# Kernel tuning notes

Hardware: AMD Instinct MI355X
Metric: run time of the kernel (lower is better)

The kernel has to match this reference:

```python
import jax, jax.numpy as jnp
import numpy as np

EPS = 1e-5

def _gru(m, h, wih, whh, bih, bhh):
    gi = m @ wih.T + bih
    gh = h @ whh.T + bhh
    ir, iz, inn = jnp.split(gi, 3, axis=-1)
    hr, hz, hn = jnp.split(gh, 3, axis=-1)
    r = jax.nn.sigmoid(ir + hr)
    z = jax.nn.sigmoid(iz + hz)
    n = jnp.tanh(inn + r * hn)
    return (1.0 - z) * n + z * h

def _mggc(h, src, dst, etype, coeff, w, wih, whh, bih, bhh, num_nodes):
    # w: [L, T, C, C]; per-edge-type linear transform, scatter-add aggregation, GRU update
    for l in range(w.shape[0]):
        tr = jnp.einsum('nc,tcd->tnd', h, w[l])            # [T, N, C]
        msg = tr[etype, src] * coeff[src][:, None]          # [E, C] gather by (edge type, source)
        aggr = jax.ops.segment_sum(msg, dst, num_segments=num_nodes)
        h = _gru(aggr, h, wih, whh, bih, bhh)
    return h

def _bn(x, g, b):
    mu = x.mean(axis=0)
    var = x.var(axis=0)
    return (x - mu) * jax.lax.rsqrt(var + EPS) * g + b

def _lstm_cell(inp, h, c, wih, whh, b):
    gates = inp @ wih.T + h @ whh.T + b
    i, f, g, o = jnp.split(gates, 4, axis=-1)
    c = jax.nn.sigmoid(f) * c + jax.nn.sigmoid(i) * jnp.tanh(g)
    h = jax.nn.sigmoid(o) * jnp.tanh(c)
    return h, c

def _set2set(x, batch, num_graphs, wih0, whh0, b0, wih1, whh1, b1, steps=5):
    C = x.shape[1]
    B = num_graphs
    q_star = jnp.zeros((B, 2 * C), x.dtype)
    h0 = jnp.zeros((B, C), x.dtype); c0 = h0; h1 = h0; c1 = h0
    for _ in range(steps):
        h0, c0 = _lstm_cell(q_star, h0, c0, wih0, whh0, b0)
        h1, c1 = _lstm_cell(h0, h1, c1, wih1, whh1, b1)
        q = h1                                              # [B, C]
        e = jnp.sum(x * q[batch], axis=-1)                  # [N]
        emax = jax.ops.segment_max(e, batch, num_segments=B)
        ex = jnp.exp(e - emax[batch])
        denom = jax.ops.segment_sum(ex, batch, num_segments=B)
        a = ex / denom[batch]                               # scatter-softmax over graphs
        r = jax.ops.segment_sum(a[:, None] * x, batch, num_segments=B)
        q_star = jnp.concatenate([q, r], axis=1)
    return q_star                                           # [B, 2C]

def _forward(x, edge_attr, conv_w, conv_wih, conv_whh, conv_bih, conv_bhh, conv_nt,
             s2s1_wih0, s2s1_whh0, s2s1_b0, s2s1_wih1, s2s1_whh1, s2s1_b1,
             s2s2_wih0, s2s2_whh0, s2s2_b0, s2s2_wih1, s2s2_whh1, s2s2_b1,
             bn_g, bn_b, prebn_g, prebn_b,
             fc_w0, fc_b0, fc_w1, fc_b1, fc_w2, fc_b2,
             fcbn_g0, fcbn_b0, fcbn_g1, fcbn_b1,
             edge_index, node_type, batch, assign_src, assign_dst, edge_index_2, batch_2, num_graphs):
    N = x.shape[0]
    N2 = batch_2.shape[0]
    etype = jnp.argmax(edge_attr[:, :4], axis=1)           # edge type from one-hot part of edge_attr
    src, dst = edge_index[0], edge_index[1]
    h = x
    for i in range(3):
        coeff = conv_nt[i][node_type]                      # per-node-type coefficient
        h = _mggc(h, src, dst, etype, coeff, conv_w[i], conv_wih[i], conv_whh[i], conv_bih[i], conv_bhh[i], N)
        h = jax.nn.relu(_bn(h, bn_g[i], bn_b[i]))
    x1 = _set2set(h, batch, num_graphs, s2s1_wih0, s2s1_whh0, s2s1_b0, s2s1_wih1, s2s1_whh1, s2s1_b1)
    # avg_pool: mean of level-1 node features into level-2 clusters
    cnt = jax.ops.segment_sum(jnp.ones((assign_dst.shape[0],), x.dtype), assign_dst, num_segments=N2)
    h2 = jax.ops.segment_sum(h[assign_src], assign_dst, num_segments=N2) / jnp.maximum(cnt, 1.0)[:, None]
    src2, dst2 = edge_index_2[0], edge_index_2[1]
    etype2 = jnp.zeros((src2.shape[0],), jnp.int32)
    ones2 = jnp.ones((N2,), x.dtype)
    h2 = jax.nn.relu(_mggc(h2, src2, dst2, etype2, ones2, conv_w[3], conv_wih[3], conv_whh[3], conv_bih[3], conv_bhh[3], N2))
    h2 = jax.nn.relu(_mggc(h2, src2, dst2, etype2, ones2, conv_w[4], conv_wih[4], conv_whh[4], conv_bih[4], conv_bhh[4], N2))
    x2 = _set2set(h2, batch_2, num_graphs, s2s2_wih0, s2s2_whh0, s2s2_b0, s2s2_wih1, s2s2_whh1, s2s2_b1)
    z = jnp.concatenate([x1, x2], axis=1)                  # [B, 4C] = [B, 256]
    z = _bn(z, prebn_g, prebn_b)
    z = jax.nn.relu(_bn(z @ fc_w0.T + fc_b0, fcbn_g0, fcbn_b0))  # dropout: eval-mode identity
    z = jax.nn.relu(_bn(z @ fc_w1.T + fc_b1, fcbn_g1, fcbn_b1))
    return z @ fc_w2.T + fc_b2                             # [B, 1]

def setup_inputs() -> dict:
    C, L, T, NT = 64, 3, 4, 9
    N, E, N2, E2, A, B = 60000, 600000, 20000, 150000, 60000, 256
    key = jax.random.key(0)
    ks = iter(jax.random.split(key, 48))
    nrm = lambda shape, s: jax.random.normal(next(ks), shape, jnp.float32) * s
    inp = {}
    inp['x'] = nrm((N, C), 1.0)
    inp['edge_attr'] = jax.random.uniform(next(ks), (E, 10), jnp.float32)
    inp['conv_w'] = nrm((5, L, T, C, C), 0.125)
    inp['conv_wih'] = nrm((5, 3 * C, C), 0.125)
    inp['conv_whh'] = nrm((5, 3 * C, C), 0.125)
    inp['conv_bih'] = jnp.zeros((5, 3 * C), jnp.float32)
    inp['conv_bhh'] = jnp.zeros((5, 3 * C), jnp.float32)
    inp['conv_nt'] = 1.0 + nrm((5, NT), 0.1)
    for nm in ('s2s1', 's2s2'):
        inp[nm + '_wih0'] = nrm((4 * C, 2 * C), 0.09)
        inp[nm + '_whh0'] = nrm((4 * C, C), 0.125)
        inp[nm + '_b0'] = jnp.zeros((4 * C,), jnp.float32)
        inp[nm + '_wih1'] = nrm((4 * C, C), 0.125)
        inp[nm + '_whh1'] = nrm((4 * C, C), 0.125)
        inp[nm + '_b1'] = jnp.zeros((4 * C,), jnp.float32)
    inp['bn_g'] = jnp.ones((3, C), jnp.float32)
    inp['bn_b'] = jnp.zeros((3, C), jnp.float32)
    inp['prebn_g'] = jnp.ones((4 * C,), jnp.float32)
    inp['prebn_b'] = jnp.zeros((4 * C,), jnp.float32)
    inp['fc_w0'] = nrm((128, 256), 0.0625)
    inp['fc_b0'] = jnp.zeros((128,), jnp.float32)
    inp['fc_w1'] = nrm((64, 128), 0.09)
    inp['fc_b1'] = jnp.zeros((64,), jnp.float32)
    inp['fc_w2'] = nrm((1, 64), 0.125)
    inp['fc_b2'] = jnp.zeros((1,), jnp.float32)
    inp['fcbn_g0'] = jnp.ones((128,), jnp.float32)
    inp['fcbn_b0'] = jnp.zeros((128,), jnp.float32)
    inp['fcbn_g1'] = jnp.ones((64,), jnp.float32)
    inp['fcbn_b1'] = jnp.zeros((64,), jnp.float32)
    inp['edge_index'] = jax.random.randint(next(ks), (2, E), 0, N)
    inp['node_type'] = jax.random.randint(next(ks), (N,), 0, NT)
    inp['batch'] = jnp.sort(jax.random.randint(next(ks), (N,), 0, B))
    inp['assign_src'] = jax.random.randint(next(ks), (A,), 0, N)
    inp['assign_dst'] = jax.random.randint(next(ks), (A,), 0, N2)
    inp['edge_index_2'] = jax.random.randint(next(ks), (2, E2), 0, N2)
    inp['batch_2'] = jnp.sort(jax.random.randint(next(ks), (N2,), 0, B))
    inp['num_graphs'] = B
    return inp

def reference(x, edge_attr, conv_w, conv_wih, conv_whh, conv_bih, conv_bhh, conv_nt,
              s2s1_wih0, s2s1_whh0, s2s1_b0, s2s1_wih1, s2s1_whh1, s2s1_b1,
              s2s2_wih0, s2s2_whh0, s2s2_b0, s2s2_wih1, s2s2_whh1, s2s2_b1,
              bn_g, bn_b, prebn_g, prebn_b,
              fc_w0, fc_b0, fc_w1, fc_b1, fc_w2, fc_b2,
              fcbn_g0, fcbn_b0, fcbn_g1, fcbn_b1,
              edge_index, node_type, batch, assign_src, assign_dst, edge_index_2, batch_2, num_graphs):
    return _forward(x, edge_attr, conv_w, conv_wih, conv_whh, conv_bih, conv_bhh, conv_nt,
                    s2s1_wih0, s2s1_whh0, s2s1_b0, s2s1_wih1, s2s1_whh1, s2s1_b1,
                    s2s2_wih0, s2s2_whh0, s2s2_b0, s2s2_wih1, s2s2_whh1, s2s2_b1,
                    bn_g, bn_b, prebn_g, prebn_b,
                    fc_w0, fc_b0, fc_w1, fc_b1, fc_w2, fc_b2,
                    fcbn_g0, fcbn_b0, fcbn_g1, fcbn_b1,
                    edge_index, node_type, batch, assign_src, assign_dst, edge_index_2, batch_2, num_graphs)
```

## Files before the change

kernel.cpp:

```cpp
#include <hip/hip_runtime.h>

#define NN1 60000
#define EE1 600000
#define NN2 20000
#define EE2 150000
#define AA  60000

__device__ __forceinline__ float sigf(float x){ return 1.f/(1.f+expf(-x)); }
__device__ __forceinline__ float rlane(float v, int sl){
  return __int_as_float(__builtin_amdgcn_readlane(__float_as_int(v), sl));
}
#define RL4(SL) hx = rlane(ld.x, SL); hy = rlane(ld.y, SL); hz = rlane(ld.z, SL); hw = rlane(ld.w, SL);
#define FMA4(A, W) A = fmaf(hx, W.x, A); A = fmaf(hy, W.y, A); A = fmaf(hz, W.z, A); A = fmaf(hw, W.w, A);

__global__ void k_relu(float* a, int n){
  int i = blockIdx.x*blockDim.x + threadIdx.x;
  if (i < n) a[i] = fmaxf(a[i], 0.f);
}
__global__ void k_copy(const float* __restrict__ a, float* __restrict__ o, int n){
  int i = blockIdx.x*blockDim.x + threadIdx.x;
  if (i < n) o[i] = a[i];
}

__global__ void k_etype(const float* __restrict__ ea, int* __restrict__ etype, int E){
  int e = blockIdx.x*blockDim.x + threadIdx.x;
  if (e >= E) return;
  const float* p = ea + (size_t)e*10;
  float best = p[0]; int bi = 0;
  #pragma unroll
  for (int k = 1; k < 4; ++k){ float v = p[k]; if (v > best){ best = v; bi = k; } }
  etype[e] = bi;
}

__global__ void k_coeff(const float* __restrict__ nt, const int* __restrict__ node_type,
                        float* __restrict__ coeff, int N){
  int n = blockIdx.x*blockDim.x + threadIdx.x;
  if (n < N) coeff[n] = nt[node_type[n]];
}

__global__ void k_batchptr(const int* __restrict__ batch, int* __restrict__ rb, int N, int B){
  int n = blockIdx.x*blockDim.x + threadIdx.x;
  if (n >= N) return;
  int b = batch[n];
  if (n == 0){ for (int g = 0; g <= b; ++g) rb[g] = 0; }
  else {
    int pb = batch[n-1];
    for (int g = pb+1; g <= b; ++g) rb[g] = n;
  }
  if (n == N-1){ for (int g = b+1; g <= B; ++g) rb[g] = N; }
}

__global__ void k_prep_msgw(const float* __restrict__ w, float* __restrict__ w4){
  int idx = blockIdx.x*256 + threadIdx.x;
  if (idx >= 245760) return;
  int m = idx >> 12, r = idx & 4095;
  int c4 = r >> 8, d = (r >> 2) & 63, q = r & 3;
  w4[idx] = w[m*4096 + (4*c4+q)*64 + d];
}
__global__ void k_prep_gruw(const float* __restrict__ wih, const float* __restrict__ whh,
                            float* __restrict__ wihT, float* __restrict__ wihW,
                            float* __restrict__ whh4){
  int idx = blockIdx.x*256 + threadIdx.x;
  if (idx >= 61440) return;
  {
    int l = idx / 12288, r = idx % 12288;
    int t = r >> 12, rr = r & 4095;
    int c4 = rr >> 8, d = (rr >> 2) & 63, q = rr & 3;
    wihT[idx] = wih[l*12288 + (64*t + d)*64 + 4*c4 + q];
  }
  {
    int l = idx / 12288, rr = idx % 12288;
    int e = rr >> 2, q = rr & 3;
    int c4 = e / 192, j = e - c4*192;
    wihW[idx] = wih[l*12288 + j*64 + 4*c4 + q];
    whh4[idx] = whh[l*12288 + j*64 + 4*c4 + q];
  }
}

__global__ void k_s2strans(const float* __restrict__ wih0, const float* __restrict__ whh0,
                           const float* __restrict__ wih1, const float* __restrict__ whh1,
                           float* __restrict__ T){
  int idx = blockIdx.x*256 + threadIdx.x;
  if (idx < 32768){ int k = idx >> 8, j = idx & 255; T[idx] = wih0[j*128 + k]; }
  else if (idx < 49152){ int r = idx - 32768; int k = r >> 8, j = r & 255; T[idx] = whh0[j*64 + k]; }
  else if (idx < 65536){ int r = idx - 49152; int k = r >> 8, j = r & 255; T[idx] = wih1[j*64 + k]; }
  else if (idx < 81920){ int r = idx - 65536; int k = r >> 8, j = r & 255; T[idx] = whh1[j*64 + k]; }
}

__global__ void k_hist(const int* __restrict__ dst, int* __restrict__ cnt, int E){
  int e = blockIdx.x*blockDim.x + threadIdx.x;
  if (e >= E) return;
  atomicAdd(&cnt[dst[e]], 1);
}
__global__ void k_chunksum(const int* __restrict__ cnt, int* __restrict__ csum, int M){
  __shared__ int sh[256];
  int base = blockIdx.x*1024;
  int s = 0;
  for (int i = threadIdx.x; i < 1024; i += 256){
    int idx = base + i;
    if (idx < M) s += cnt[idx];
  }
  sh[threadIdx.x] = s;
  __syncthreads();
  for (int o = 128; o; o >>= 1){
    if (threadIdx.x < o) sh[threadIdx.x] += sh[threadIdx.x + o];
    __syncthreads();
  }
  if (threadIdx.x == 0) csum[blockIdx.x] = sh[0];
}
__global__ void k_chunkscan(int* __restrict__ csum, int nchunk){
  __shared__ int sh[256];
  int i = threadIdx.x;
  int v = (i < nchunk) ? csum[i] : 0;
  sh[i] = v; __syncthreads();
  for (int o = 1; o < 256; o <<= 1){
    int y = (i >= o) ? sh[i-o] : 0;
    __syncthreads();
    sh[i] += y;
    __syncthreads();
  }
  if (i < nchunk) csum[i] = sh[i] - v;
  if (i == 255) csum[nchunk] = sh[255];
}
__global__ void k_chunkapply(const int* __restrict__ cnt, const int* __restrict__ csum,
                             int* __restrict__ R, int* __restrict__ cur, int M){
  __shared__ int sh[256];
  int base = blockIdx.x*1024;
  int i0 = base + threadIdx.x*4;
  int v[4]; int s = 0;
  #pragma unroll
  for (int k = 0; k < 4; ++k){ int idx = i0 + k; v[k] = (idx < M) ? cnt[idx] : 0; s += v[k]; }
  sh[threadIdx.x] = s; __syncthreads();
  for (int o = 1; o < 256; o <<= 1){
    int y = (threadIdx.x >= o) ? sh[threadIdx.x-o] : 0;
    __syncthreads();
    sh[threadIdx.x] += y;
    __syncthreads();
  }
  int run = csum[blockIdx.x] + sh[threadIdx.x] - s;
  #pragma unroll
  for (int k = 0; k < 4; ++k){
    int idx = i0 + k;
    if (idx < M){ R[idx] = run; cur[idx] = run; run += v[k]; }
  }
  if (threadIdx.x == 255 && base + 1024 >= M) R[M] = csum[blockIdx.x] + sh[255];
}
__global__ void k_scatter(const int* __restrict__ src, const int* __restrict__ dst,
                          const int* __restrict__ etype, int* __restrict__ cur,
                          int* __restrict__ ep, int E){
  int e = blockIdx.x*blockDim.x + threadIdx.x;
  if (e >= E) return;
  int t = etype ? etype[e] : 0;
  int pos = atomicAdd(&cur[dst[e]], 1);
  ep[pos] = (t << 20) | src[e];
}


__global__ __launch_bounds__(1024, 4) void k_tr4d(
    const float* __restrict__ h, const float* __restrict__ W4,
    const float* __restrict__ coeff, float* __restrict__ tr, int N){
  extern __shared__ float4 wl[];
  for (int i = threadIdx.x; i < 4096; i += 1024) wl[i] = ((const float4*)W4)[i];
  __syncthreads();
  int lane = threadIdx.x & 63, wv = threadIdx.x >> 6;
  int ng = N >> 2, stride = gridDim.x*16;
  for (int g = blockIdx.x*16 + wv; g < ng; g += stride){
    int n0 = g << 2;
    float4 ld = ((const float4*)(h + ((size_t)n0 << 6)))[lane];
    float a00=0.f,a01=0.f,a02=0.f,a03=0.f;
    float a10=0.f,a11=0.f,a12=0.f,a13=0.f;
    float a20=0.f,a21=0.f,a22=0.f,a23=0.f;
    float a30=0.f,a31=0.f,a32=0.f,a33=0.f;
    for (int c4 = 0; c4 < 16; ++c4){
      int wb = (c4 << 6) + lane;
      float4 w0 = wl[wb], w1 = wl[1024+wb], w2 = wl[2048+wb], w3 = wl[3072+wb];
      float hx, hy, hz, hw;
      RL4(c4)     FMA4(a00,w0) FMA4(a10,w1) FMA4(a20,w2) FMA4(a30,w3)
      RL4(16|c4)  FMA4(a01,w0) FMA4(a11,w1) FMA4(a21,w2) FMA4(a31,w3)
      RL4(32|c4)  FMA4(a02,w0) FMA4(a12,w1) FMA4(a22,w2) FMA4(a32,w3)
      RL4(48|c4)  FMA4(a03,w0) FMA4(a13,w1) FMA4(a23,w2) FMA4(a33,w3)
    }
    float4 cv = ((const float4*)coeff)[g];
    a00*=cv.x; a01*=cv.y; a02*=cv.z; a03*=cv.w;
    a10*=cv.x; a11*=cv.y; a12*=cv.z; a13*=cv.w;
    a20*=cv.x; a21*=cv.y; a22*=cv.z; a23*=cv.w;
    a30*=cv.x; a31*=cv.y; a32*=cv.z; a33*=cv.w;
    float* o0 = tr + ((size_t)n0 << 6) + lane;
    o0[0]=a00; o0[64]=a01; o0[128]=a02; o0[192]=a03;
    float* o1 = tr + (((size_t)N + n0) << 6) + lane;
    o1[0]=a10; o1[64]=a11; o1[128]=a12; o1[192]=a13;
    float* o2 = tr + (((size_t)2*N + n0) << 6) + lane;
    o2[0]=a20; o2[64]=a21; o2[128]=a22; o2[192]=a23;
    float* o3 = tr + (((size_t)3*N + n0) << 6) + lane;
    o3[0]=a30; o3[64]=a31; o3[128]=a32; o3[192]=a33;
  }
}

__global__ __launch_bounds__(256) void k_tr1(
    const float* __restrict__ h, const float* __restrict__ W4,
    const float* __restrict__ coeff, float* __restrict__ tr, int N){
  __shared__ float4 wl[1024];
  for (int i = threadIdx.x; i < 1024; i += 256) wl[i] = ((const float4*)W4)[i];
  __syncthreads();
  int lane = threadIdx.x & 63, w = threadIdx.x >> 6;
  int ng = N >> 2, stride = gridDim.x*4;
  for (int g = blockIdx.x*4 + w; g < ng; g += stride){
    int n0 = g << 2;
    float4 ld = ((const float4*)(h + ((size_t)n0 << 6)))[lane];
    float a0=0.f, a1=0.f, a2=0.f, a3=0.f;
    for (int c4 = 0; c4 < 16; ++c4){
      float4 w0 = wl[(c4 << 6) + lane];
      float hx, hy, hz, hw;
      RL4(c4)       FMA4(a0, w0)
      RL4(16|c4)    FMA4(a1, w0)
      RL4(32|c4)    FMA4(a2, w0)
      RL4(48|c4)    FMA4(a3, w0)
    }
    if (coeff){
      float4 cv = ((const float4*)coeff)[g];
      a0 *= cv.x; a1 *= cv.y; a2 *= cv.z; a3 *= cv.w;
    }
    float* o0 = tr + ((size_t)n0 << 6) + lane;
    o0[0] = a0; o0[64] = a1; o0[128] = a2; o0[192] = a3;
  }
}

__global__ void k_sweep_p(const float* __restrict__ tr, const int* __restrict__ R,
                          const int* __restrict__ ep, float* __restrict__ aggr, int N){
  int w = threadIdx.x >> 6, lane = threadIdx.x & 63;
  int d = blockIdx.x*4 + w;
  if (d >= N) return;
  int p = R[d], pend = R[d+1];
  float acc = 0.f;
  while (p < pend){
    int m = pend - p; if (m > 64) m = 64;
    int ev = (lane < m) ? ep[p + lane] : 0;
    for (int j = 0; j < m; ++j){
      int pk = __shfl(ev, j);
      int s = pk & 0xFFFFF, t = pk >> 20;
      acc += tr[((size_t)t*N + s)*64 + lane];
    }
    p += m;
  }
  aggr[(size_t)d*64 + lane] = acc;
}

__global__ __launch_bounds__(256) void k_tr3(
    const float* __restrict__ h, const float* __restrict__ W4,
    float* __restrict__ tr, int N){
  __shared__ float4 wl[3072];
  for (int i = threadIdx.x; i < 3072; i += 256) wl[i] = ((const float4*)W4)[i];
  __syncthreads();
  int lane = threadIdx.x & 63, w = threadIdx.x >> 6;
  int ng = N >> 2, stride = gridDim.x*4;
  for (int g = blockIdx.x*4 + w; g < ng; g += stride){
    int n0 = g << 2;
    float4 ld = ((const float4*)(h + ((size_t)n0 << 6)))[lane];
    float a00=0.f,a01=0.f,a02=0.f,a03=0.f;
    float a10=0.f,a11=0.f,a12=0.f,a13=0.f;
    float a20=0.f,a21=0.f,a22=0.f,a23=0.f;
    for (int c4 = 0; c4 < 16; ++c4){
      float4 w0 = wl[(c4 << 6) + lane];
      float4 w1 = wl[1024 + (c4 << 6) + lane];
      float4 w2 = wl[2048 + (c4 << 6) + lane];
      float hx, hy, hz, hw;
      RL4(c4)       FMA4(a00, w0) FMA4(a10, w1) FMA4(a20, w2)
      RL4(16|c4)    FMA4(a01, w0) FMA4(a11, w1) FMA4(a21, w2)
      RL4(32|c4)    FMA4(a02, w0) FMA4(a12, w1) FMA4(a22, w2)
      RL4(48|c4)    FMA4(a03, w0) FMA4(a13, w1) FMA4(a23, w2)
    }
    float* o0 = tr + ((size_t)n0 << 6) + lane;
    o0[0] = a00; o0[64] = a01; o0[128] = a02; o0[192] = a03;
    float* o1 = tr + (((size_t)N + n0) << 6) + lane;
    o1[0] = a10; o1[64] = a11; o1[128] = a12; o1[192] = a13;
    float* o2 = tr + (((size_t)2*N + n0) << 6) + lane;
    o2[0] = a20; o2[64] = a21; o2[128] = a22; o2[192] = a23;
  }
}

#define RLAH(SL) \
  ax = rlane(la.x, SL); ay = rlane(la.y, SL); az2 = rlane(la.z, SL); aw = rlane(la.w, SL); \
  hx = rlane(ld.x, SL); hy = rlane(ld.y, SL); hz  = rlane(ld.z, SL); hw = rlane(ld.w, SL);
#define GACC(SL, R, Z, P, Q) RLAH(SL) \
  R = fmaf(ax,iwr.x,R); R = fmaf(ay,iwr.y,R); R = fmaf(az2,iwr.z,R); R = fmaf(aw,iwr.w,R); \
  R = fmaf(hx,hwr.x,R); R = fmaf(hy,hwr.y,R); R = fmaf(hz,hwr.z,R);  R = fmaf(hw,hwr.w,R); \
  Z = fmaf(ax,iwz.x,Z); Z = fmaf(ay,iwz.y,Z); Z = fmaf(az2,iwz.z,Z); Z = fmaf(aw,iwz.w,Z); \
  Z = fmaf(hx,hwz.x,Z); Z = fmaf(hy,hwz.y,Z); Z = fmaf(hz,hwz.z,Z);  Z = fmaf(hw,hwz.w,Z); \
  P = fmaf(ax,iwn.x,P); P = fmaf(ay,iwn.y,P); P = fmaf(az2,iwn.z,P); P = fmaf(aw,iwn.w,P); \
  Q = fmaf(hx,hwn.x,Q); Q = fmaf(hy,hwn.y,Q); Q = fmaf(hz,hwn.z,Q);  Q = fmaf(hw,hwn.w,Q);
#define GFIN(K, R, Z, P, Q) { \
    size_t off = base + ((size_t)(K) << 6) + lane; \
    float hv = h[off]; \
    float r = sigf(R), z = sigf(Z); \
    float nn = tanhf(P + r*Q); \
    h[off] = (1.f - z)*nn + z*hv; }
__global__ __launch_bounds__(1024, 4) void k_gru_fused(
    const float* __restrict__ aggr, float* __restrict__ h,
    const float* __restrict__ wihW, const float* __restrict__ whhW,
    const float* __restrict__ bih, const float* __restrict__ bhh, int N){
  extern __shared__ float4 wl[];
  for (int i = threadIdx.x; i < 6144; i += 1024)
    wl[i] = (i < 3072) ? ((const float4*)wihW)[i] : ((const float4*)whhW)[i - 3072];
  __syncthreads();
  const float4* wi = wl;
  const float4* wh = wl + 3072;
  int lane = threadIdx.x & 63, wv = threadIdx.x >> 6;
  float br  = bih[lane]     + bhh[lane];
  float bz  = bih[64+lane]  + bhh[64+lane];
  float bp  = bih[128+lane];
  float bq  = bhh[128+lane];
  int ng = N >> 2, stride = gridDim.x*16;
  for (int g = blockIdx.x*16 + wv; g < ng; g += stride){
    int n0 = g << 2;
    size_t base = (size_t)n0 << 6;
    float4 la = ((const float4*)(aggr + base))[lane];
    float4 ld = ((const float4*)(h + base))[lane];
    float r0=br, r1=br, r2=br, r3=br;
    float z0=bz, z1=bz, z2=bz, z3=bz;
    float p0=bp, p1=bp, p2=bp, p3=bp;
    float q0=bq, q1=bq, q2=bq, q3=bq;
    for (int c4 = 0; c4 < 16; ++c4){
      int wb = c4*192 + lane;
      float4 iwr = wi[wb], iwz = wi[wb+64], iwn = wi[wb+128];
      float4 hwr = wh[wb], hwz = wh[wb+64], hwn = wh[wb+128];
      float ax, ay, az2, aw, hx, hy, hz, hw;
      GACC(c4,    r0, z0, p0, q0)
      GACC(16|c4, r1, z1, p1, q1)
      GACC(32|c4, r2, z2, p2, q2)
      GACC(48|c4, r3, z3, p3, q3)
    }
    GFIN(0, r0, z0, p0, q0)
    GFIN(1, r1, z1, p1, q1)
    GFIN(2, r2, z2, p2, q2)
    GFIN(3, r3, z3, p3, q3)
  }
}

#define GRUACC(SL, RK, ZK, NK) RL4(SL) FMA4(RK, wr) FMA4(ZK, wz) FMA4(NK, wn)
#define GRUFIN(K, RK, ZK, NK) { \
    size_t off = base + (K << 6) + lane; \
    float gir = gi[off], giz = gi[S + off], gin = gi[2*S + off]; \
    float hv = h[off]; \
    float r = sigf(gir + bir + RK); \
    float z = sigf(giz + biz + ZK); \
    float nv = tanhf(gin + bin_ + r*NK); \
    h[off] = (1.f - z)*nv + z*hv; }
__global__ __launch_bounds__(256, 3) void k_gru_finW(
    const float* __restrict__ gi, float* __restrict__ h,
    const float* __restrict__ whh4,
    const float* __restrict__ bih, const float* __restrict__ bhh, int N){
  __shared__ float4 wh[3072];
  for (int i = threadIdx.x; i < 3072; i += 256) wh[i] = ((const float4*)whh4)[i];
  __syncthreads();
  int lane = threadIdx.x & 63, w = threadIdx.x >> 6;
  float bir = bih[lane], biz = bih[64+lane], bin_ = bih[128+lane];
  float bhr = bhh[lane], bhz = bhh[64+lane], bhn = bhh[128+lane];
  size_t S = (size_t)N << 6;
  int ng = N >> 2, stride = gridDim.x*4;
  for (int g = blockIdx.x*4 + w; g < ng; g += stride){
    int n0 = g << 2;
    size_t base = (size_t)n0 << 6;
    float4 ld = ((const float4*)(h + base))[lane];
    float ar0=bhr, ar1=bhr, ar2=bhr, ar3=bhr;
    float az0=bhz, az1=bhz, az2=bhz, az3=bhz;
    float an0=bhn, an1=bhn, an2=bhn, an3=bhn;
    for (int c4 = 0; c4 < 16; ++c4){
      int wb = c4*192 + lane;
      float4 wr = wh[wb];
      float4 wz = wh[wb + 64];
      float4 wn = wh[wb + 128];
      float hx, hy, hz, hw;
      GRUACC(c4,    ar0, az0, an0)
      GRUACC(16|c4, ar1, az1, an1)
      GRUACC(32|c4, ar2, az2, an2)
      GRUACC(48|c4, ar3, az3, an3)
    }
    GRUFIN(0, ar0, az0, an0)
    GRUFIN(1, ar1, az1, an1)
    GRUFIN(2, ar2, az2, an2)
    GRUFIN(3, ar3, az3, an3)
  }
}

__global__ void k_bnstats(const float* __restrict__ h, float* __restrict__ stats, int N){
  int c = threadIdx.x & 63;
  int g = threadIdx.x >> 6;
  float s = 0.f, s2 = 0.f;
  for (int n = blockIdx.x*4 + g; n < N; n += gridDim.x*4){
    float v = h[(size_t)n*64 + c]; s += v; s2 += v*v;
  }
  __shared__ float sh[4][64], sh2[4][64];
  sh[g][c] = s; sh2[g][c] = s2;
  __syncthreads();
  if (g == 0){
    float ts = sh[0][c]+sh[1][c]+sh[2][c]+sh[3][c];
    float t2 = sh2[0][c]+sh2[1][c]+sh2[2][c]+sh2[3][c];
    atomicAdd(&stats[c], ts); atomicAdd(&stats[64+c], t2);
  }
}
__global__ void k_bnapply(float* __restrict__ h, const float* __restrict__ stats,
                          const float* __restrict__ g, const float* __restrict__ b,
                          int N, int relu){
  int i = blockIdx.x*blockDim.x + threadIdx.x;
  if (i >= N*64) return;
  int c = i & 63;
  float inv = 1.f/(float)N;
  float mean = stats[c]*inv;
  float var  = stats[64+c]*inv - mean*mean;
  float y = (h[i]-mean)*rsqrtf(var + 1e-5f)*g[c] + b[c];
  if (relu) y = fmaxf(y, 0.f);
  h[i] = y;
}

__global__ void k_pool_acc(const float* __restrict__ h, const int* __restrict__ asrc,
                           const int* __restrict__ adst, float* __restrict__ h2,
                           float* __restrict__ cnt, int A){
  int i = blockIdx.x*blockDim.x + threadIdx.x;
  if (i >= A*64) return;
  int a = i >> 6, c = i & 63;
  int s = asrc[a], d = adst[a];
  atomicAdd(&h2[(size_t)d*64 + c], h[(size_t)s*64 + c]);
  if (c == 0) atomicAdd(&cnt[d], 1.f);
}
__global__ void k_pool_div(float* __restrict__ h2, const float* __restrict__ cnt, int N){
  int i = blockIdx.x*blockDim.x + threadIdx.x;
  if (i >= N*64) return;
  h2[i] = h2[i] / fmaxf(cnt[i >> 6], 1.f);
}

__global__ __launch_bounds__(1024) void k_set2set(const float* __restrict__ x, const int* __restrict__ rb,
                          const float* __restrict__ T,
                          const float* __restrict__ b0, const float* __restrict__ b1,
                          float* __restrict__ xout){
  int b = blockIdx.x, j = threadIdx.x;
  int w = j >> 6, lane = j & 63;
  __shared__ float qstar[128], h0[64], c0[64], h1[64], c1[64];
  __shared__ float gs[256], wmax[16], wsum[16], racc[16][64];
  if (j < 128) qstar[j] = 0.f;
  if (j < 64){ h0[j] = 0.f; c0[j] = 0.f; h1[j] = 0.f; c1[j] = 0.f; }
  __syncthreads();
  int n0 = rb[b], n1 = rb[b+1];
  const float* T0 = T;
  const float* T1 = T + 32768;
  const float* T2 = T + 49152;
  const float* T3 = T + 65536;
  for (int s = 0; s < 5; ++s){
    if (j < 256){
      float a0 = b0[j], a1 = 0.f, a2 = 0.f, a3 = 0.f;
      #pragma unroll 4
      for (int k = 0; k < 128; k += 4){
        a0 = fmaf(T0[(k+0)*256 + j], qstar[k+0], a0);
        a1 = fmaf(T0[(k+1)*256 + j], qstar[k+1], a1);
        a2 = fmaf(T0[(k+2)*256 + j], qstar[k+2], a2);
        a3 = fmaf(T0[(k+3)*256 + j], qstar[k+3], a3);
      }
      #pragma unroll 4
      for (int k = 0; k < 64; k += 4){
        a0 = fmaf(T1[(k+0)*256 + j], h0[k+0], a0);
        a1 = fmaf(T1[(k+1)*256 + j], h0[k+1], a1);
        a2 = fmaf(T1[(k+2)*256 + j], h0[k+2], a2);
        a3 = fmaf(T1[(k+3)*256 + j], h0[k+3], a3);
      }
      gs[j] = (a0 + a1) + (a2 + a3);
    }
    __syncthreads();
    if (j < 64){
      float ig = sigf(gs[j]);
      float fg = sigf(gs[64+j]);
      float gg = tanhf(gs[128+j]);
      float og = sigf(gs[192+j]);
      float cn = fg*c0[j] + ig*gg;
      c0[j] = cn;
      h0[j] = og*tanhf(cn);
    }
    __syncthreads();
    if (j < 256){
      float a0 = b1[j], a1 = 0.f, a2 = 0.f, a3 = 0.f;
      #pragma unroll 4
      for (int k = 0; k < 64; k += 4){
        a0 = fmaf(T2[(k+0)*256 + j], h0[k+0], a0);
        a1 = fmaf(T2[(k+1)*256 + j], h0[k+1], a1);
        a2 = fmaf(T2[(k+2)*256 + j], h0[k+2], a2);
        a3 = fmaf(T2[(k+3)*256 + j], h0[k+3], a3);
      }
      #pragma unroll 4
      for (int k = 0; k < 64; k += 4){
        a0 = fmaf(T3[(k+0)*256 + j], h1[k+0], a0);
        a1 = fmaf(T3[(k+1)*256 + j], h1[k+1], a1);
        a2 = fmaf(T3[(k+2)*256 + j], h1[k+2], a2);
        a3 = fmaf(T3[(k+3)*256 + j], h1[k+3], a3);
      }
      gs[j] = (a0 + a1) + (a2 + a3);
    }
    __syncthreads();
    if (j < 64){
      float ig = sigf(gs[j]);
      float fg = sigf(gs[64+j]);
      float gg = tanhf(gs[128+j]);
      float og = sigf(gs[192+j]);
      float cn = fg*c1[j] + ig*gg;
      c1[j] = cn;
      float hn = og*tanhf(cn);
      h1[j] = hn;
      qstar[j] = hn;
    }
    __syncthreads();
    float lmax = -3.4e38f;
    for (int n = n0 + w; n < n1; n += 16){
      float v = x[(size_t)n*64 + lane]*qstar[lane];
      #pragma unroll
      for (int o = 32; o; o >>= 1) v += __shfl_xor(v, o);
      lmax = fmaxf(lmax, v);
    }
    if (lane == 0) wmax[w] = lmax;
    __syncthreads();
    float bmax = wmax[0];
    #pragma unroll
    for (int k = 1; k < 16; ++k) bmax = fmaxf(bmax, wmax[k]);
    float lsum = 0.f, lr = 0.f;
    for (int n = n0 + w; n < n1; n += 16){
      float xv = x[(size_t)n*64 + lane];
      float v = xv*qstar[lane];
      #pragma unroll
      for (int o = 32; o; o >>= 1) v += __shfl_xor(v, o);
      float wexp = expf(v - bmax);
      lsum += wexp;
      lr = fmaf(wexp, xv, lr);
    }
    if (lane == 0) wsum[w] = lsum;
    racc[w][lane] = lr;
    __syncthreads();
    if (j < 64){
      float r = 0.f, denom = 0.f;
      #pragma unroll
      for (int k = 0; k < 16; ++k){ r += racc[k][j]; denom += wsum[k]; }
      qstar[64 + j] = (denom > 0.f) ? (r/denom) : 0.f;
    }
    __syncthreads();
  }
  if (j < 128) xout[(size_t)b*128 + j] = qstar[j];
}

__global__ void k_concat(const float* __restrict__ x1, const float* __restrict__ x2,
                         float* __restrict__ z){
  int i = blockIdx.x*blockDim.x + threadIdx.x;
  if (i >= 256*256) return;
  int b = i >> 8, c = i & 255;
  z[i] = (c < 128) ? x1[b*128 + c] : x2[b*128 + (c - 128)];
}
__global__ void k_bn_par(float* __restrict__ X, const float* __restrict__ g,
                         const float* __restrict__ b, int F, int relu){
  int f = blockIdx.x, i = threadIdx.x;
  float v = X[(size_t)i*F + f];
  __shared__ float s1[256], s2[256];
  s1[i] = v; s2[i] = v*v;
  __syncthreads();
  for (int o = 128; o; o >>= 1){
    if (i < o){ s1[i] += s1[i+o]; s2[i] += s2[i+o]; }
    __syncthreads();
  }
  float mean = s1[0]*(1.f/256.f);
  float var  = s2[0]*(1.f/256.f) - mean*mean;
  float y = (v - mean)*rsqrtf(var + 1e-5f)*g[f] + b[f];
  if (relu) y = fmaxf(y, 0.f);
  X[(size_t)i*F + f] = y;
}
__global__ void k_fc(const float* __restrict__ X, const float* __restrict__ W,
                     const float* __restrict__ bias, float* __restrict__ Y, int K, int F){
  int b = blockIdx.x, f = threadIdx.x;
  if (f >= F) return;
  const float* xr = X + (size_t)b*K;
  const float* wr = W + (size_t)f*K;
  float acc = bias[f];
  for (int k = 0; k < K; ++k) acc = fmaf(xr[k], wr[k], acc);
  Y[(size_t)b*F + f] = acc;
}
__global__ void k_fc_out(const float* __restrict__ z2, const float* __restrict__ w,
                         const float* __restrict__ bias, float* __restrict__ out){
  int b = blockIdx.x*blockDim.x + threadIdx.x;
  if (b >= 256) return;
  float acc = bias[0];
  #pragma unroll
  for (int k = 0; k < 64; ++k) acc = fmaf(z2[b*64 + k], w[k], acc);
  out[b] = acc;
}

extern "C" void kernel_launch(void* const* d_in, const int* in_sizes, int n_in,
                              void* d_out, int out_size, void* d_ws, size_t ws_size,
                              hipStream_t stream) {
  const float* x_in     = (const float*)d_in[0];
  const float* edge_attr= (const float*)d_in[1];
  const float* conv_w   = (const float*)d_in[2];
  const float* conv_wih = (const float*)d_in[3];
  const float* conv_whh = (const float*)d_in[4];
  const float* conv_bih = (const float*)d_in[5];
  const float* conv_bhh = (const float*)d_in[6];
  const float* conv_nt  = (const float*)d_in[7];
  const float* s1_wih0 = (const float*)d_in[8];
  const float* s1_whh0 = (const float*)d_in[9];
  const float* s1_b0   = (const float*)d_in[10];
  const float* s1_wih1 = (const float*)d_in[11];
  const float* s1_whh1 = (const float*)d_in[12];
  const float* s1_b1   = (const float*)d_in[13];
  const float* s2_wih0 = (const float*)d_in[14];
  const float* s2_whh0 = (const float*)d_in[15];
  const float* s2_b0   = (const float*)d_in[16];
  const float* s2_wih1 = (const float*)d_in[17];
  const float* s2_whh1 = (const float*)d_in[18];
  const float* s2_b1   = (const float*)d_in[19];
  const float* bn_g    = (const float*)d_in[20];
  const float* bn_b    = (const float*)d_in[21];
  const float* prebn_g = (const float*)d_in[22];
  const float* prebn_b = (const float*)d_in[23];
  const float* fc_w0   = (const float*)d_in[24];
  const float* fc_b0   = (const float*)d_in[25];
  const float* fc_w1   = (const float*)d_in[26];
  const float* fc_b1   = (const float*)d_in[27];
  const float* fc_w2   = (const float*)d_in[28];
  const float* fc_b2   = (const float*)d_in[29];
  const float* fcbn_g0 = (const float*)d_in[30];
  const float* fcbn_b0 = (const float*)d_in[31];
  const float* fcbn_g1 = (const float*)d_in[32];
  const float* fcbn_b1 = (const float*)d_in[33];
  const int* edge_index   = (const int*)d_in[34];
  const int* node_type    = (const int*)d_in[35];
  const int* batch        = (const int*)d_in[36];
  const int* assign_src   = (const int*)d_in[37];
  const int* assign_dst   = (const int*)d_in[38];
  const int* edge_index_2 = (const int*)d_in[39];
  const int* batch_2      = (const int*)d_in[40];
  (void)in_sizes; (void)n_in; (void)out_size; (void)ws_size;

  int fused_ok = (hipFuncSetAttribute((const void*)k_gru_fused,
                    hipFuncAttributeMaxDynamicSharedMemorySize, 98304) == hipSuccess);
  int tr4_ok = (hipFuncSetAttribute((const void*)k_tr4d,
                    hipFuncAttributeMaxDynamicSharedMemorySize, 65536) == hipSuccess);

  float* Wp = (float*)d_ws;
  size_t o = 0;
  auto alloc = [&](size_t n){ float* p = Wp + o; o += n; return p; };
  float* h     = alloc((size_t)NN1*64);
  float* tr    = alloc((size_t)4*NN1*64);
  float* aggr  = alloc((size_t)NN1*64);
  float* coeff = alloc(NN1);
  float* h2    = alloc((size_t)NN2*64);
  float* cnt   = alloc(NN2);
  float* x1    = alloc(256*128);
  float* x2    = alloc(256*128);
  float* z     = alloc(256*256);
  float* z1    = alloc(256*128);
  float* z2    = alloc(256*64);
  float* stats = alloc(128);
  float* w4    = alloc(245760);
  float* wihT  = alloc(61440);
  float* wihW  = alloc(61440);
  float* whh4  = alloc(61440);
  float* s2sT1 = alloc(81920);
  float* s2sT2 = alloc(81920);
  int* etype = (int*)alloc(EE1);
  int* cnt1  = (int*)alloc(NN1);
  int* R1    = (int*)alloc(NN1 + 1);
  int* ep1   = (int*)alloc(EE1);
  int* cnt2  = (int*)alloc(NN2);
  int* R2    = (int*)alloc(NN2 + 1);
  int* ep2   = (int*)alloc(EE2);
  int* csum  = (int*)alloc(260);
  int* rb1   = (int*)alloc(257);
  int* rb2   = (int*)alloc(257);

  const int* src1 = edge_index;
  const int* dst1 = edge_index + EE1;
  const int* src2 = edge_index_2;
  const int* dst2 = edge_index_2 + EE2;

  k_etype<<<(EE1+255)/256, 256, 0, stream>>>(edge_attr, etype, EE1);
  k_copy<<<(NN1*64+255)/256, 256, 0, stream>>>(x_in, h, NN1*64);
  k_prep_msgw<<<(245760+255)/256, 256, 0, stream>>>(conv_w, w4);
  k_prep_gruw<<<(61440+255)/256, 256, 0, stream>>>(conv_wih, conv_whh, wihT, wihW, whh4);
  k_s2strans<<<(81920+255)/256, 256, 0, stream>>>(s1_wih0, s1_whh0, s1_wih1, s1_whh1, s2sT1);
  k_s2strans<<<(81920+255)/256, 256, 0, stream>>>(s2_wih0, s2_whh0, s2_wih1, s2_whh1, s2sT2);
  k_batchptr<<<(NN1+255)/256, 256, 0, stream>>>(batch, rb1, NN1, 256);
  k_batchptr<<<(NN2+255)/256, 256, 0, stream>>>(batch_2, rb2, NN2, 256);

  {
    int M = NN1, nchunk = (M + 1023)/1024;
    hipMemsetAsync(cnt1, 0, (size_t)M*sizeof(int), stream);
    k_hist<<<(EE1+255)/256, 256, 0, stream>>>(dst1, cnt1, EE1);
    k_chunksum<<<nchunk, 256, 0, stream>>>(cnt1, csum, M);
    k_chunkscan<<<1, 256, 0, stream>>>(csum, nchunk);
    k_chunkapply<<<nchunk, 256, 0, stream>>>(cnt1, csum, R1, cnt1, M);
    k_scatter<<<(EE1+255)/256, 256, 0, stream>>>(src1, dst1, etype, cnt1, ep1, EE1);
  }
  {
    int M = NN2, nchunk = (M + 1023)/1024;
    hipMemsetAsync(cnt2, 0, (size_t)M*sizeof(int), stream);
    k_hist<<<(EE2+255)/256, 256, 0, stream>>>(dst2, cnt2, EE2);
    k_chunksum<<<nchunk, 256, 0, stream>>>(cnt2, csum, M);
    k_chunkscan<<<1, 256, 0, stream>>>(csum, nchunk);
    k_chunkapply<<<nchunk, 256, 0, stream>>>(cnt2, csum, R2, cnt2, M);
    k_scatter<<<(EE2+255)/256, 256, 0, stream>>>(src2, dst2, nullptr, cnt2, ep2, EE2);
  }

  auto gru = [&](float* hbuf, int N, int lidx){
    if (fused_ok){
      k_gru_fused<<<256, 1024, 98304, stream>>>(aggr, hbuf,
          wihW + (size_t)lidx*12288, whh4 + (size_t)lidx*12288,
          conv_bih + lidx*192, conv_bhh + lidx*192, N);
    } else {
      k_tr3<<<768, 256, 0, stream>>>(aggr, wihT + (size_t)lidx*12288, tr, N);
      k_gru_finW<<<768, 256, 0, stream>>>(tr, hbuf, whh4 + (size_t)lidx*12288,
          conv_bih + lidx*192, conv_bhh + lidx*192, N);
    }
  };

  for (int i = 0; i < 3; ++i){
    k_coeff<<<(NN1+255)/256, 256, 0, stream>>>(conv_nt + i*9, node_type, coeff, NN1);
    for (int l = 0; l < 3; ++l){
      const float* W4l = w4 + (size_t)(i*3+l)*16384;
      if (tr4_ok){
        k_tr4d<<<512, 1024, 65536, stream>>>(h, W4l, coeff, tr, NN1);
      } else {
        for (int t = 0; t < 4; ++t)
          k_tr1<<<1024, 256, 0, stream>>>(h, W4l + (size_t)t*4096, coeff,
                                          tr + (size_t)t*NN1*64, NN1);
      }
      k_sweep_p<<<(NN1+3)/4, 256, 0, stream>>>(tr, R1, ep1, aggr, NN1);
      gru(h, NN1, i);
    }
    hipMemsetAsync(stats, 0, 128*sizeof(float), stream);
    k_bnstats<<<256, 256, 0, stream>>>(h, stats, NN1);
    k_bnapply<<<(NN1*64+255)/256, 256, 0, stream>>>(h, stats, bn_g + i*64, bn_b + i*64, NN1, 1);
  }

  k_set2set<<<256, 1024, 0, stream>>>(h, rb1, s2sT1, s1_b0, s1_b1, x1);

  hipMemsetAsync(h2, 0, (size_t)NN2*64*sizeof(float), stream);
  hipMemsetAsync(cnt, 0, (size_t)NN2*sizeof(float), stream);
  k_pool_acc<<<(AA*64+255)/256, 256, 0, stream>>>(h, assign_src, assign_dst, h2, cnt, AA);
  k_pool_div<<<(NN2*64+255)/256, 256, 0, stream>>>(h2, cnt, NN2);

  for (int L = 3; L < 5; ++L){
    for (int l = 0; l < 3; ++l){
      const float* W4l = w4 + (size_t)(L*3+l)*16384;
      k_tr1<<<1250, 256, 0, stream>>>(h2, W4l, nullptr, tr, NN2);
      k_sweep_p<<<(NN2+3)/4, 256, 0, stream>>>(tr, R2, ep2, aggr, NN2);
      gru(h2, NN2, L);
    }
    k_relu<<<(NN2*64+255)/256, 256, 0, stream>>>(h2, NN2*64);
  }

  k_set2set<<<256, 1024, 0, stream>>>(h2, rb2, s2sT2, s2_b0, s2_b1, x2);

  k_concat<<<256, 256, 0, stream>>>(x1, x2, z);
  k_bn_par<<<256, 256, 0, stream>>>(z, prebn_g, prebn_b, 256, 0);
  k_fc<<<256, 128, 0, stream>>>(z, fc_w0, fc_b0, z1, 256, 128);
  k_bn_par<<<128, 256, 0, stream>>>(z1, fcbn_g0, fcbn_b0, 128, 1);
  k_fc<<<256, 64, 0, stream>>>(z1, fc_w1, fc_b1, z2, 128, 64);
  k_bn_par<<<64, 256, 0, stream>>>(z2, fcbn_g1, fcbn_b1, 64, 1);
  k_fc_out<<<4, 64, 0, stream>>>(z2, fc_w2, fc_b2, (float*)d_out);
}
```

Baseline: 2.398 ms.

## Unroll CSR gather with precomputed row indices and single-pass online softmax in set2set

Each edge entry now stores a precomputed row index (type*N + src), so the sweep kernel no longer unpacks the type and source fields. The gather loop is unrolled by four with independent accumulators to keep more loads in flight. The set2set attention loop becomes a single-pass online softmax with per-wave max/sum rescaling, which avoids reading x twice and removes one block barrier. The cost is extra exp calls per node and per-wave rescaling, and floating-point summation order changes slightly.

Result: faster. 2.192 ms (-8.6%).

```diff
diff --git a/kernel.cpp b/kernel.cpp
--- a/kernel.cpp
+++ b/kernel.cpp
@@ -147,12 +147,12 @@
 }
 __global__ void k_scatter(const int* __restrict__ src, const int* __restrict__ dst,
                           const int* __restrict__ etype, int* __restrict__ cur,
-                          int* __restrict__ ep, int E){
+                          int* __restrict__ ep, int E, int N){
   int e = blockIdx.x*blockDim.x + threadIdx.x;
   if (e >= E) return;
   int t = etype ? etype[e] : 0;
   int pos = atomicAdd(&cur[dst[e]], 1);
-  ep[pos] = (t << 20) | src[e];
+  ep[pos] = t*N + src[e];
 }
 
 
@@ -231,18 +231,27 @@
   int d = blockIdx.x*4 + w;
   if (d >= N) return;
   int p = R[d], pend = R[d+1];
-  float acc = 0.f;
+  float a0=0.f, a1=0.f, a2=0.f, a3=0.f;
   while (p < pend){
     int m = pend - p; if (m > 64) m = 64;
     int ev = (lane < m) ? ep[p + lane] : 0;
-    for (int j = 0; j < m; ++j){
-      int pk = __shfl(ev, j);
-      int s = pk & 0xFFFFF, t = pk >> 20;
-      acc += tr[((size_t)t*N + s)*64 + lane];
+    int j = 0;
+    for (; j + 4 <= m; j += 4){
+      int r0 = __shfl(ev, j),   r1 = __shfl(ev, j+1);
+      int r2 = __shfl(ev, j+2), r3 = __shfl(ev, j+3);
+      float v0 = tr[((size_t)r0 << 6) + lane];
+      float v1 = tr[((size_t)r1 << 6) + lane];
+      float v2 = tr[((size_t)r2 << 6) + lane];
+      float v3 = tr[((size_t)r3 << 6) + lane];
+      a0 += v0; a1 += v1; a2 += v2; a3 += v3;
+    }
+    for (; j < m; ++j){
+      int r0 = __shfl(ev, j);
+      a0 += tr[((size_t)r0 << 6) + lane];
     }
     p += m;
   }
-  aggr[(size_t)d*64 + lane] = acc;
+  aggr[(size_t)d*64 + lane] = (a0 + a1) + (a2 + a3);
 }
 
 __global__ __launch_bounds__(256) void k_tr3(
@@ -505,35 +514,33 @@
       qstar[j] = hn;
     }
     __syncthreads();
-    float lmax = -3.4e38f;
-    for (int n = n0 + w; n < n1; n += 16){
-      float v = x[(size_t)n*64 + lane]*qstar[lane];
-      #pragma unroll
-      for (int o = 32; o; o >>= 1) v += __shfl_xor(v, o);
-      lmax = fmaxf(lmax, v);
-    }
-    if (lane == 0) wmax[w] = lmax;
-    __syncthreads();
-    float bmax = wmax[0];
-    #pragma unroll
-    for (int k = 1; k < 16; ++k) bmax = fmaxf(bmax, wmax[k]);
-    float lsum = 0.f, lr = 0.f;
+    float lmax = -3.4e38f, lsum = 0.f, lr = 0.f;
     for (int n = n0 + w; n < n1; n += 16){
       float xv = x[(size_t)n*64 + lane];
       float v = xv*qstar[lane];
       #pragma unroll
       for (int o = 32; o; o >>= 1) v += __shfl_xor(v, o);
-      float wexp = expf(v - bmax);
-      lsum += wexp;
-      lr = fmaf(wexp, xv, lr);
-    }
-    if (lane == 0) wsum[w] = lsum;
+      float nm = fmaxf(lmax, v);
+      float corr = expf(lmax - nm);
+      float e = expf(v - nm);
+      lsum = fmaf(lsum, corr, e);
+      lr   = fmaf(lr, corr, e*xv);
+      lmax = nm;
+    }
+    if (lane == 0){ wmax[w] = lmax; wsum[w] = lsum; }
     racc[w][lane] = lr;
     __syncthreads();
     if (j < 64){
-      float r = 0.f, denom = 0.f;
+      float M = wmax[0];
       #pragma unroll
-      for (int k = 0; k < 16; ++k){ r += racc[k][j]; denom += wsum[k]; }
+      for (int k = 1; k < 16; ++k) M = fmaxf(M, wmax[k]);
+      float denom = 0.f, r = 0.f;
+      #pragma unroll
+      for (int k = 0; k < 16; ++k){
+        float sc = expf(wmax[k] - M);
+        denom = fmaf(wsum[k], sc, denom);
+        r     = fmaf(racc[k][j], sc, r);
+      }
       qstar[64 + j] = (denom > 0.f) ? (r/denom) : 0.f;
     }
     __syncthreads();
@@ -689,7 +696,7 @@
     k_chunksum<<<nchunk, 256, 0, stream>>>(cnt1, csum, M);
     k_chunkscan<<<1, 256, 0, stream>>>(csum, nchunk);
     k_chunkapply<<<nchunk, 256, 0, stream>>>(cnt1, csum, R1, cnt1, M);
-    k_scatter<<<(EE1+255)/256, 256, 0, stream>>>(src1, dst1, etype, cnt1, ep1, EE1);
+    k_scatter<<<(EE1+255)/256, 256, 0, stream>>>(src1, dst1, etype, cnt1, ep1, EE1, NN1);
   }
   {
     int M = NN2, nchunk = (M + 1023)/1024;
@@ -698,7 +705,7 @@
     k_chunksum<<<nchunk, 256, 0, stream>>>(cnt2, csum, M);
     k_chunkscan<<<1, 256, 0, stream>>>(csum, nchunk);
     k_chunkapply<<<nchunk, 256, 0, stream>>>(cnt2, csum, R2, cnt2, M);
-    k_scatter<<<(EE2+255)/256, 256, 0, stream>>>(src2, dst2, nullptr, cnt2, ep2, EE2);
+    k_scatter<<<(EE2+255)/256, 256, 0, stream>>>(src2, dst2, nullptr, cnt2, ep2, EE2, NN2);
   }
 
   auto gru = [&](float* hbuf, int N, int lidx){
```
